# Performance work log

Measured on AMD Instinct MI355X. Metric: run time of the kernel, lower is better.

The kernel has to match this reference:

```python
import jax, jax.numpy as jnp
import numpy as np

NUM_HEAD = 16

def setup_inputs() -> dict:
    rk = jax.random.key(0)
    k1, k2, k3, k4, k5 = jax.random.split(rk, 5)
    B, Sq, Skv, D = 4, 2048, 2048, 1024
    return {
        "query": jax.random.normal(k1, (B, Sq, D), dtype=jnp.float32),
        "key":   jax.random.normal(k2, (B, Skv, D), dtype=jnp.float32),
        "value": jax.random.normal(k3, (B, Skv, D), dtype=jnp.float32),
        "W": jax.random.normal(k4, (D, D), dtype=jnp.float32) * (D ** -0.5),
        "b": jax.random.normal(k5, (D,), dtype=jnp.float32) * 0.01,
    }

def reference(query, key, value, W, b):
    B, Sq, D = query.shape
    H = NUM_HEAD
    hd = D // H
    # chunk(num_head, -1) == split last dim into H contiguous heads
    q = query.reshape(B, Sq, H, hd)
    k = key.reshape(B, -1, H, hd)
    v = value.reshape(B, -1, H, hd)
    # scores[b,h,q,k] = (Q_h K_h^T) / sqrt(embedding_dim)  (full dim, per source)
    scores = jnp.einsum('bqhd,bkhd->bhqk', q, k) / jnp.sqrt(jnp.float32(D))
    # nn.Softmax(dim=1) on a [B, q, kv] matrix -> softmax over the QUERY axis
    attn = jax.nn.softmax(scores, axis=2)
    out = jnp.einsum('bhqk,bkhd->bqhd', attn, v).reshape(B, Sq, D)
    # final linear: x @ W^T + b
    return out @ W.T + b
```

## Files before the change

### kernel.cpp

```cpp
#include <hip/hip_runtime.h>

#define NH    16
#define HD    64
#define SQ    2048
#define SKV   2048
#define DM    1024

typedef __attribute__((ext_vector_type(8))) __bf16 bf16x8;
typedef __attribute__((ext_vector_type(4))) __bf16 bf16x4;
typedef __attribute__((ext_vector_type(4))) float  f32x4;
typedef __attribute__((ext_vector_type(4))) short  s16x4;

#define ASYNC16(gp, lp)                                                        \
    __builtin_amdgcn_global_load_lds(                                          \
        (const __attribute__((address_space(1))) void*)(gp),                   \
        (__attribute__((address_space(3))) void*)(lp), 16, 0, 0)

#if __has_builtin(__builtin_amdgcn_exp2f)
#define EXPS(x) __builtin_amdgcn_exp2f((x) * 0.04508422f)
#else
#define EXPS(x) __expf((x) * 0.03125f)
#endif

#if __has_builtin(__builtin_amdgcn_mfma_f32_16x16x16bf16_1k)
static __device__ __forceinline__ f32x4 mfma16(bf16x4 a, bf16x4 b, f32x4 c) {
    return __builtin_amdgcn_mfma_f32_16x16x16bf16_1k(
        __builtin_bit_cast(s16x4, a), __builtin_bit_cast(s16x4, b), c, 0, 0, 0);
}
#else
static __device__ __forceinline__ f32x4 mfma16(bf16x4 a, bf16x4 b, f32x4 c) {
    asm volatile("s_nop 1\n\tv_mfma_f32_16x16x16_bf16 %0, %1, %2, %0"
                 : "+v"(c) : "v"(a), "v"(b));
    return c;
}
#endif

static __device__ __forceinline__ int swz(int row, int chunk) {
    return (row << 6) + (((chunk) ^ (row & 7)) << 3);
}

static __device__ __forceinline__ bf16x4 cvt4(float4 v) {
    bf16x4 r;
    r[0] = (__bf16)v.x; r[1] = (__bf16)v.y; r[2] = (__bf16)v.z; r[3] = (__bf16)v.w;
    return r;
}

__global__ void kprep_all(const float* __restrict__ q, const float* __restrict__ k,
                          const float* __restrict__ W,
                          __bf16* __restrict__ Qh, __bf16* __restrict__ Kh,
                          __bf16* __restrict__ Wb) {
    int bid = blockIdx.x;
    if (bid < 8192) {
        const float* src = (bid < 4096) ? q : k;
        __bf16* dst = (bid < 4096) ? Qh : Kh;
        size_t g = (size_t)(bid & 4095) * 256 + threadIdx.x;
        size_t o = g * 8;
        int c  = (int)(o & 63);
        int s  = (int)((o >> 6) & 2047);
        int bh = (int)(o >> 17);
        int b = bh >> 4, h = bh & 15;
        const float* p = src + ((size_t)(b * SQ + s)) * DM + h * HD + c;
        float4 v0 = *(const float4*)p;
        float4 v1 = *(const float4*)(p + 4);
        bf16x8 r;
        r[0] = (__bf16)v0.x; r[1] = (__bf16)v0.y; r[2] = (__bf16)v0.z; r[3] = (__bf16)v0.w;
        r[4] = (__bf16)v1.x; r[5] = (__bf16)v1.y; r[6] = (__bf16)v1.z; r[7] = (__bf16)v1.w;
        *(bf16x8*)(dst + o) = r;
    } else {
        int i = (bid - 8192) * 256 + threadIdx.x;
        float4 v = *(const float4*)(W + (size_t)i * 4);
        *(bf16x4*)(Wb + (size_t)i * 4) = cvt4(v);
    }
}

__global__ __launch_bounds__(256, 4) void kz(const __bf16* __restrict__ Qh,
                                             const __bf16* __restrict__ Kh,
                                             const float* __restrict__ v,
                                             __bf16* __restrict__ Vt) {
    const int bh = blockIdx.x;
    const int kb = blockIdx.y;
    const int b = bh >> 4, h = bh & 15;
    const int t = threadIdx.x;
    const int w = t >> 6, lane = t & 63;
    const int lo16 = lane & 15, quad = lane >> 4;
    const int wub = (t & 192) << 3;

    __shared__ __bf16 Ks[128 * 64];
    __shared__ __bf16 Qs[2][64 * 64];
    __shared__ float  Zs[128];

    const __bf16* kbase = Kh + ((size_t)bh * SKV + kb * 128) * HD;
    const __bf16* qbase = Qh + (size_t)bh * SQ * HD;

#pragma unroll
    for (int i = 0; i < 4; ++i) {
        int ci = i * 256 + t;
        int row = ci >> 3;
        int c = (ci & 7) ^ (row & 7);
        ASYNC16(kbase + row * 64 + c * 8, &Ks[i * 2048 + wub]);
    }
#pragma unroll
    for (int i = 0; i < 2; ++i) {
        int ci = i * 256 + t;
        int row = ci >> 3;
        int c = (ci & 7) ^ (row & 7);
        ASYNC16(qbase + row * 64 + c * 8, &Qs[0][i * 2048 + wub]);
    }
    __syncthreads();

    bf16x8 bk[2][2];
#pragma unroll
    for (int nt = 0; nt < 2; ++nt)
#pragma unroll
        for (int dh = 0; dh < 2; ++dh)
            bk[nt][dh] = *(const bf16x8*)(&Ks[swz(w * 32 + nt * 16 + lo16, dh * 4 + quad)]);

    float zacc[2] = {0.f, 0.f};

    for (int qt = 0; qt < 32; ++qt) {
        const int cur = qt & 1, nxt = cur ^ 1;
        if (qt < 31) {
#pragma unroll
            for (int i = 0; i < 2; ++i) {
                int ci = i * 256 + t;
                int row = ci >> 3;
                int c = (ci & 7) ^ (row & 7);
                ASYNC16(qbase + (size_t)(qt + 1) * 64 * HD + row * 64 + c * 8,
                        &Qs[nxt][i * 2048 + wub]);
            }
        }

#pragma unroll
        for (int mt = 0; mt < 4; ++mt) {
            bf16x8 aq0 = *(const bf16x8*)(&Qs[cur][swz(mt * 16 + lo16, quad)]);
            bf16x8 aq1 = *(const bf16x8*)(&Qs[cur][swz(mt * 16 + lo16, 4 + quad)]);
#pragma unroll
            for (int nt = 0; nt < 2; ++nt) {
                f32x4 acc = {0.f, 0.f, 0.f, 0.f};
                acc = __builtin_amdgcn_mfma_f32_16x16x32_bf16(aq0, bk[nt][0], acc, 0, 0, 0);
                acc = __builtin_amdgcn_mfma_f32_16x16x32_bf16(aq1, bk[nt][1], acc, 0, 0, 0);
                zacc[nt] += EXPS(acc[0]) + EXPS(acc[1]) + EXPS(acc[2]) + EXPS(acc[3]);
            }
        }
        __syncthreads();
    }

#pragma unroll
    for (int nt = 0; nt < 2; ++nt) {
        float s = zacc[nt];
        s += __shfl_xor(s, 16, 64);
        s += __shfl_xor(s, 32, 64);
        if (lane < 16) Zs[w * 32 + nt * 16 + lane] = s;
    }
    __syncthreads();

    {
        int kk = t & 127, dh2 = t >> 7;
        float rz = 1.0f / Zs[kk];
        int kfull = kb * 128 + kk;
        const float* vrow = v + ((size_t)(b * SKV) + kfull) * DM + h * HD + dh2 * 32;
        size_t vtb = (size_t)bh * HD * SKV + (size_t)(dh2 * 32) * SKV + kfull;
#pragma unroll
        for (int dc = 0; dc < 2; ++dc) {
            float4 a0 = *(const float4*)(vrow + dc * 16 + 0);
            float4 a1 = *(const float4*)(vrow + dc * 16 + 4);
            float4 a2 = *(const float4*)(vrow + dc * 16 + 8);
            float4 a3 = *(const float4*)(vrow + dc * 16 + 12);
            float tmp[16] = {a0.x, a0.y, a0.z, a0.w, a1.x, a1.y, a1.z, a1.w,
                             a2.x, a2.y, a2.z, a2.w, a3.x, a3.y, a3.z, a3.w};
#pragma unroll
            for (int j = 0; j < 16; ++j)
                Vt[vtb + (size_t)(dc * 16 + j) * SKV] = (__bf16)(tmp[j] * rz);
        }
    }
}

__global__ __launch_bounds__(256, 2) void kattn(const __bf16* __restrict__ Qh,
                                                const __bf16* __restrict__ Kh,
                                                const __bf16* __restrict__ Vt,
                                                __bf16* __restrict__ O) {
    const int bh = blockIdx.x;
    const int qb = blockIdx.y;
    const int b = bh >> 4, h = bh & 15;
    const int t = threadIdx.x;
    const int w = t >> 6, lane = t & 63;
    const int lo16 = lane & 15, quad = lane >> 4;
    const int wub = (t & 192) << 3;

    __shared__ __bf16 Ks[2][64 * 64];
    __shared__ __bf16 Vts[2][64 * 64];
    __shared__ __bf16 Qstage[256 * 64];

    const __bf16* qgbase = Qh + ((size_t)bh * SQ + qb * 256) * HD;
    const __bf16* kgbase = Kh + (size_t)bh * SKV * HD;
    const __bf16* vtgbase = Vt + (size_t)bh * HD * SKV;

#pragma unroll
    for (int i = 0; i < 8; ++i) {
        int ci = i * 256 + t;
        int row = ci >> 3;
        int c = (ci & 7) ^ (row & 7);
        ASYNC16(qgbase + row * 64 + c * 8, &Qstage[i * 2048 + wub]);
    }
#pragma unroll
    for (int i = 0; i < 2; ++i) {
        int ci = i * 256 + t;
        int row = ci >> 3;
        int c = (ci & 7) ^ (row & 7);
        ASYNC16(kgbase + row * 64 + c * 8, &Ks[0][i * 2048 + wub]);
        ASYNC16(vtgbase + (size_t)row * SKV + c * 8, &Vts[0][i * 2048 + wub]);
    }
    __syncthreads();

    bf16x8 qf[4][2];
#pragma unroll
    for (int qt = 0; qt < 4; ++qt)
#pragma unroll
        for (int dh = 0; dh < 2; ++dh)
            qf[qt][dh] = *(const bf16x8*)(&Qstage[swz(w * 64 + qt * 16 + lo16, dh * 4 + quad)]);

    f32x4 oacc[4][4];
    f32x4 zero = {0.f, 0.f, 0.f, 0.f};
#pragma unroll
    for (int qt = 0; qt < 4; ++qt)
#pragma unroll
        for (int nt = 0; nt < 4; ++nt)
            oacc[qt][nt] = zero;

    for (int kt = 0; kt < 32; ++kt) {
        const int cur = kt & 1, nxt = cur ^ 1;
        if (kt < 31) {
#pragma unroll
            for (int i = 0; i < 2; ++i) {
                int ci = i * 256 + t;
                int row = ci >> 3;
                int c = (ci & 7) ^ (row & 7);
                ASYNC16(kgbase + (size_t)(kt + 1) * 64 * HD + row * 64 + c * 8,
                        &Ks[nxt][i * 2048 + wub]);
                ASYNC16(vtgbase + (size_t)row * SKV + (kt + 1) * 64 + c * 8,
                        &Vts[nxt][i * 2048 + wub]);
            }
        }

        bf16x4 ef[4][4];
#pragma unroll
        for (int kg = 0; kg < 4; ++kg) {
            bf16x8 ak0 = *(const bf16x8*)(&Ks[cur][swz(kg * 16 + lo16, quad)]);
            bf16x8 ak1 = *(const bf16x8*)(&Ks[cur][swz(kg * 16 + lo16, 4 + quad)]);
#pragma unroll
            for (int qt = 0; qt < 4; ++qt) {
                f32x4 s = zero;
                s = __builtin_amdgcn_mfma_f32_16x16x32_bf16(ak0, qf[qt][0], s, 0, 0, 0);
                s = __builtin_amdgcn_mfma_f32_16x16x32_bf16(ak1, qf[qt][1], s, 0, 0, 0);
                bf16x4 e;
                e[0] = (__bf16)EXPS(s[0]);
                e[1] = (__bf16)EXPS(s[1]);
                e[2] = (__bf16)EXPS(s[2]);
                e[3] = (__bf16)EXPS(s[3]);
                ef[qt][kg] = e;
            }
        }

#pragma unroll
        for (int nt = 0; nt < 4; ++nt) {
#pragma unroll
            for (int kg = 0; kg < 4; ++kg) {
                int row = nt * 16 + lo16;
                int chunk = kg * 2 + (quad >> 1);
                bf16x4 bv = *(const bf16x4*)(
                    &Vts[cur][(row << 6) + ((chunk ^ (row & 7)) << 3) + ((quad & 1) << 2)]);
#pragma unroll
                for (int qt = 0; qt < 4; ++qt)
                    oacc[qt][nt] = mfma16(ef[qt][kg], bv, oacc[qt][nt]);
            }
        }
        __syncthreads();
    }

    asm volatile("s_nop 7\n\ts_nop 7" ::: );

    size_t obase = ((size_t)(b * SQ) + qb * 256 + w * 64) * DM + h * HD;
#pragma unroll
    for (int qt = 0; qt < 4; ++qt)
#pragma unroll
        for (int nt = 0; nt < 4; ++nt)
#pragma unroll
            for (int r = 0; r < 4; ++r)
                O[obase + (size_t)(qt * 16 + quad * 4 + r) * DM + nt * 16 + lo16] =
                    (__bf16)oacc[qt][nt][r];
}

__global__ __launch_bounds__(256, 2) void kproj(const __bf16* __restrict__ A,
                                                const __bf16* __restrict__ Wb,
                                                const float* __restrict__ bias,
                                                float* __restrict__ out) {
    const int nb = blockIdx.x;
    const int mb = blockIdx.y;
    const int t = threadIdx.x;
    const int w = t >> 6, lane = t & 63;
    const int lo16 = lane & 15, quad = lane >> 4;
    const int wm = w & 1, wn = w >> 1;
    const int wub = (t & 192) << 3;

    __shared__ __bf16 As[2][128 * 64];
    __shared__ __bf16 Bs[2][128 * 64];

    f32x4 acc[4][4];
    f32x4 zero = {0.f, 0.f, 0.f, 0.f};
#pragma unroll
    for (int mt = 0; mt < 4; ++mt)
#pragma unroll
        for (int nt = 0; nt < 4; ++nt)
            acc[mt][nt] = zero;

    const __bf16* abase = A + (size_t)(mb * 128) * DM;
    const __bf16* wbase = Wb + (size_t)(nb * 128) * DM;

#pragma unroll
    for (int i = 0; i < 4; ++i) {
        int ci = i * 256 + t;
        int row = ci >> 3;
        int c = (ci & 7) ^ (row & 7);
        ASYNC16(abase + (size_t)row * DM + c * 8, &As[0][i * 2048 + wub]);
        ASYNC16(wbase + (size_t)row * DM + c * 8, &Bs[0][i * 2048 + wub]);
    }
    __syncthreads();

    for (int kt = 0; kt < 16; ++kt) {
        const int cur = kt & 1, nxt = cur ^ 1;
        if (kt < 15) {
#pragma unroll
            for (int i = 0; i < 4; ++i) {
                int ci = i * 256 + t;
                int row = ci >> 3;
                int c = (ci & 7) ^ (row & 7);
                ASYNC16(abase + (size_t)row * DM + (kt + 1) * 64 + c * 8, &As[nxt][i * 2048 + wub]);
                ASYNC16(wbase + (size_t)row * DM + (kt + 1) * 64 + c * 8, &Bs[nxt][i * 2048 + wub]);
            }
        }

#pragma unroll
        for (int ks = 0; ks < 2; ++ks) {
            bf16x8 av[4], bv[4];
#pragma unroll
            for (int mt = 0; mt < 4; ++mt)
                av[mt] = *(const bf16x8*)(&As[cur][swz(wm * 64 + mt * 16 + lo16, ks * 4 + quad)]);
#pragma unroll
            for (int nt = 0; nt < 4; ++nt)
                bv[nt] = *(const bf16x8*)(&Bs[cur][swz(wn * 64 + nt * 16 + lo16, ks * 4 + quad)]);
#pragma unroll
            for (int mt = 0; mt < 4; ++mt)
#pragma unroll
                for (int nt = 0; nt < 4; ++nt)
                    acc[mt][nt] = __builtin_amdgcn_mfma_f32_16x16x32_bf16(av[mt], bv[nt], acc[mt][nt], 0, 0, 0);
        }
        __syncthreads();
    }

    const int col0 = nb * 128 + wn * 64;
    const int row0 = mb * 128 + wm * 64;
#pragma unroll
    for (int nt = 0; nt < 4; ++nt) {
        float bb = bias[col0 + nt * 16 + lo16];
#pragma unroll
        for (int mt = 0; mt < 4; ++mt)
#pragma unroll
            for (int r = 0; r < 4; ++r)
                out[(size_t)(row0 + mt * 16 + quad * 4 + r) * DM + col0 + nt * 16 + lo16] =
                    acc[mt][nt][r] + bb;
    }
}

extern "C" void kernel_launch(void* const* d_in, const int* in_sizes, int n_in,
                              void* d_out, int out_size, void* d_ws, size_t ws_size,
                              hipStream_t stream) {
    const float* q    = (const float*)d_in[0];
    const float* k    = (const float*)d_in[1];
    const float* v    = (const float*)d_in[2];
    const float* W    = (const float*)d_in[3];
    const float* bias = (const float*)d_in[4];
    float* out = (float*)d_out;

    char* ws = (char*)d_ws;
    __bf16* Qh = (__bf16*)ws;
    __bf16* Kh = (__bf16*)(ws + (16u << 20));
    __bf16* Vt = (__bf16*)(ws + (32u << 20));
    __bf16* Wb = (__bf16*)(ws + (48u << 20));
    __bf16* O  = (__bf16*)(ws + (50u << 20));

    kprep_all<<<dim3(9216), 256, 0, stream>>>(q, k, W, Qh, Kh, Wb);
    kz       <<<dim3(64, 16), 256, 0, stream>>>(Qh, Kh, v, Vt);
    kattn    <<<dim3(64, 8), 256, 0, stream>>>(Qh, Kh, Vt, O);
    kproj    <<<dim3(8, 64), 256, 0, stream>>>(O, Wb, bias, out);
}
```

Baseline: 298.3 us.

## Load Q/K/V fragments directly from global into registers, drop LDS staging

The z-normalizer and attention kernels now read their MFMA operand fragments straight from global memory into registers, using ping-pong register buffers as software prefetch, instead of staging tiles in LDS with async copies and block barriers. In the attention kernel the exponentiated scores are written to a per-wave LDS region and re-read as 8-wide operands, so the PV product uses the 16x16x32 MFMA instead of the 16x16x16 one. This removes the __syncthreads per tile and the LDS staging traffic. The cost is uncoalesced global fragment loads that rely on L2/L1 reuse across waves, and higher register pressure.

```diff
diff --git a/kernel.cpp b/kernel.cpp
--- a/kernel.cpp
+++ b/kernel.cpp
@@ -9,7 +9,6 @@
 typedef __attribute__((ext_vector_type(8))) __bf16 bf16x8;
 typedef __attribute__((ext_vector_type(4))) __bf16 bf16x4;
 typedef __attribute__((ext_vector_type(4))) float  f32x4;
-typedef __attribute__((ext_vector_type(4))) short  s16x4;
 
 #define ASYNC16(gp, lp)                                                        \
     __builtin_amdgcn_global_load_lds(                                          \
@@ -20,19 +19,6 @@
 #define EXPS(x) __builtin_amdgcn_exp2f((x) * 0.04508422f)
 #else
 #define EXPS(x) __expf((x) * 0.03125f)
-#endif
-
-#if __has_builtin(__builtin_amdgcn_mfma_f32_16x16x16bf16_1k)
-static __device__ __forceinline__ f32x4 mfma16(bf16x4 a, bf16x4 b, f32x4 c) {
-    return __builtin_amdgcn_mfma_f32_16x16x16bf16_1k(
-        __builtin_bit_cast(s16x4, a), __builtin_bit_cast(s16x4, b), c, 0, 0, 0);
-}
-#else
-static __device__ __forceinline__ f32x4 mfma16(bf16x4 a, bf16x4 b, f32x4 c) {
-    asm volatile("s_nop 1\n\tv_mfma_f32_16x16x16_bf16 %0, %1, %2, %0"
-                 : "+v"(c) : "v"(a), "v"(b));
-    return c;
-}
 #endif
 
 static __device__ __forceinline__ int swz(int row, int chunk) {
@@ -83,66 +69,53 @@
     const int t = threadIdx.x;
     const int w = t >> 6, lane = t & 63;
     const int lo16 = lane & 15, quad = lane >> 4;
-    const int wub = (t & 192) << 3;
-
-    __shared__ __bf16 Ks[128 * 64];
-    __shared__ __bf16 Qs[2][64 * 64];
-    __shared__ float  Zs[128];
+
+    __shared__ float Zs[128];
 
     const __bf16* kbase = Kh + ((size_t)bh * SKV + kb * 128) * HD;
     const __bf16* qbase = Qh + (size_t)bh * SQ * HD;
 
-#pragma unroll
-    for (int i = 0; i < 4; ++i) {
-        int ci = i * 256 + t;
-        int row = ci >> 3;
-        int c = (ci & 7) ^ (row & 7);
-        ASYNC16(kbase + row * 64 + c * 8, &Ks[i * 2048 + wub]);
-    }
-#pragma unroll
-    for (int i = 0; i < 2; ++i) {
-        int ci = i * 256 + t;
-        int row = ci >> 3;
-        int c = (ci & 7) ^ (row & 7);
-        ASYNC16(qbase + row * 64 + c * 8, &Qs[0][i * 2048 + wub]);
-    }
-    __syncthreads();
-
     bf16x8 bk[2][2];
 #pragma unroll
     for (int nt = 0; nt < 2; ++nt)
 #pragma unroll
         for (int dh = 0; dh < 2; ++dh)
-            bk[nt][dh] = *(const bf16x8*)(&Ks[swz(w * 32 + nt * 16 + lo16, dh * 4 + quad)]);
+            bk[nt][dh] = *(const bf16x8*)(kbase + (size_t)(w * 32 + nt * 16 + lo16) * HD
+                                          + dh * 32 + quad * 8);
 
     float zacc[2] = {0.f, 0.f};
 
-    for (int qt = 0; qt < 32; ++qt) {
-        const int cur = qt & 1, nxt = cur ^ 1;
-        if (qt < 31) {
-#pragma unroll
-            for (int i = 0; i < 2; ++i) {
-                int ci = i * 256 + t;
-                int row = ci >> 3;
-                int c = (ci & 7) ^ (row & 7);
-                ASYNC16(qbase + (size_t)(qt + 1) * 64 * HD + row * 64 + c * 8,
-                        &Qs[nxt][i * 2048 + wub]);
-            }
-        }
-
+    bf16x8 aqA[4][2], aqB[4][2];
+#pragma unroll
+    for (int mt = 0; mt < 4; ++mt)
+#pragma unroll
+        for (int dh = 0; dh < 2; ++dh)
+            aqA[mt][dh] = *(const bf16x8*)(qbase + (size_t)(mt * 16 + lo16) * HD
+                                           + dh * 32 + quad * 8);
+
+    auto kz_tile = [&](bf16x8 (&aqc)[4][2], bf16x8 (&aqn)[4][2], int qtn) {
+#pragma unroll
+        for (int mt = 0; mt < 4; ++mt)
+#pragma unroll
+            for (int dh = 0; dh < 2; ++dh)
+                aqn[mt][dh] = *(const bf16x8*)(qbase
+                    + (size_t)(qtn * 64 + mt * 16 + lo16) * HD + dh * 32 + quad * 8);
 #pragma unroll
         for (int mt = 0; mt < 4; ++mt) {
-            bf16x8 aq0 = *(const bf16x8*)(&Qs[cur][swz(mt * 16 + lo16, quad)]);
-            bf16x8 aq1 = *(const bf16x8*)(&Qs[cur][swz(mt * 16 + lo16, 4 + quad)]);
 #pragma unroll
             for (int nt = 0; nt < 2; ++nt) {
                 f32x4 acc = {0.f, 0.f, 0.f, 0.f};
-                acc = __builtin_amdgcn_mfma_f32_16x16x32_bf16(aq0, bk[nt][0], acc, 0, 0, 0);
-                acc = __builtin_amdgcn_mfma_f32_16x16x32_bf16(aq1, bk[nt][1], acc, 0, 0, 0);
+                acc = __builtin_amdgcn_mfma_f32_16x16x32_bf16(aqc[mt][0], bk[nt][0], acc, 0, 0, 0);
+                acc = __builtin_amdgcn_mfma_f32_16x16x32_bf16(aqc[mt][1], bk[nt][1], acc, 0, 0, 0);
                 zacc[nt] += EXPS(acc[0]) + EXPS(acc[1]) + EXPS(acc[2]) + EXPS(acc[3]);
             }
         }
-        __syncthreads();
+    };
+
+    for (int qt2 = 0; qt2 < 16; ++qt2) {
+        int qt = qt2 * 2;
+        kz_tile(aqA, aqB, qt + 1);
+        kz_tile(aqB, aqA, (qt + 2 < 32) ? qt + 2 : 31);
     }
 
 #pragma unroll
@@ -185,39 +158,20 @@
     const int t = threadIdx.x;
     const int w = t >> 6, lane = t & 63;
     const int lo16 = lane & 15, quad = lane >> 4;
-    const int wub = (t & 192) << 3;
-
-    __shared__ __bf16 Ks[2][64 * 64];
-    __shared__ __bf16 Vts[2][64 * 64];
-    __shared__ __bf16 Qstage[256 * 64];
-
-    const __bf16* qgbase = Qh + ((size_t)bh * SQ + qb * 256) * HD;
-    const __bf16* kgbase = Kh + (size_t)bh * SKV * HD;
-    const __bf16* vtgbase = Vt + (size_t)bh * HD * SKV;
-
-#pragma unroll
-    for (int i = 0; i < 8; ++i) {
-        int ci = i * 256 + t;
-        int row = ci >> 3;
-        int c = (ci & 7) ^ (row & 7);
-        ASYNC16(qgbase + row * 64 + c * 8, &Qstage[i * 2048 + wub]);
-    }
-#pragma unroll
-    for (int i = 0; i < 2; ++i) {
-        int ci = i * 256 + t;
-        int row = ci >> 3;
-        int c = (ci & 7) ^ (row & 7);
-        ASYNC16(kgbase + row * 64 + c * 8, &Ks[0][i * 2048 + wub]);
-        ASYNC16(vtgbase + (size_t)row * SKV + c * 8, &Vts[0][i * 2048 + wub]);
-    }
-    __syncthreads();
+
+    __shared__ __bf16 Es[4 * 64 * 64];
+
+    const __bf16* qg  = Qh + ((size_t)bh * SQ + qb * 256) * HD;
+    const __bf16* kgl = Kh + (size_t)bh * SKV * HD;
+    const __bf16* vtg = Vt + (size_t)bh * HD * SKV;
 
     bf16x8 qf[4][2];
 #pragma unroll
     for (int qt = 0; qt < 4; ++qt)
 #pragma unroll
         for (int dh = 0; dh < 2; ++dh)
-            qf[qt][dh] = *(const bf16x8*)(&Qstage[swz(w * 64 + qt * 16 + lo16, dh * 4 + quad)]);
+            qf[qt][dh] = *(const bf16x8*)(qg + (size_t)(w * 64 + qt * 16 + lo16) * HD
+                                          + dh * 32 + quad * 8);
 
     f32x4 oacc[4][4];
     f32x4 zero = {0.f, 0.f, 0.f, 0.f};
@@ -227,57 +181,67 @@
         for (int nt = 0; nt < 4; ++nt)
             oacc[qt][nt] = zero;
 
-    for (int kt = 0; kt < 32; ++kt) {
-        const int cur = kt & 1, nxt = cur ^ 1;
-        if (kt < 31) {
-#pragma unroll
-            for (int i = 0; i < 2; ++i) {
-                int ci = i * 256 + t;
-                int row = ci >> 3;
-                int c = (ci & 7) ^ (row & 7);
-                ASYNC16(kgbase + (size_t)(kt + 1) * 64 * HD + row * 64 + c * 8,
-                        &Ks[nxt][i * 2048 + wub]);
-                ASYNC16(vtgbase + (size_t)row * SKV + (kt + 1) * 64 + c * 8,
-                        &Vts[nxt][i * 2048 + wub]);
-            }
-        }
-
-        bf16x4 ef[4][4];
+    __bf16* Ew = &Es[w * 4096];
+
+    bf16x8 akA[4][2], akB[4][2];
+#pragma unroll
+    for (int kg = 0; kg < 4; ++kg)
+#pragma unroll
+        for (int dh = 0; dh < 2; ++dh)
+            akA[kg][dh] = *(const bf16x8*)(kgl + (size_t)(kg * 16 + lo16) * HD
+                                           + dh * 32 + quad * 8);
+
+    auto attn_tile = [&](bf16x8 (&akc)[4][2], bf16x8 (&akn)[4][2], int kt, int ktn) {
+        bf16x8 bv[2][4];
+#pragma unroll
+        for (int kk2 = 0; kk2 < 2; ++kk2)
+#pragma unroll
+            for (int nt = 0; nt < 4; ++nt)
+                bv[kk2][nt] = *(const bf16x8*)(vtg + (size_t)(nt * 16 + lo16) * SKV
+                                               + kt * 64 + kk2 * 32 + quad * 8);
 #pragma unroll
         for (int kg = 0; kg < 4; ++kg) {
-            bf16x8 ak0 = *(const bf16x8*)(&Ks[cur][swz(kg * 16 + lo16, quad)]);
-            bf16x8 ak1 = *(const bf16x8*)(&Ks[cur][swz(kg * 16 + lo16, 4 + quad)]);
 #pragma unroll
             for (int qt = 0; qt < 4; ++qt) {
                 f32x4 s = zero;
-                s = __builtin_amdgcn_mfma_f32_16x16x32_bf16(ak0, qf[qt][0], s, 0, 0, 0);
-                s = __builtin_amdgcn_mfma_f32_16x16x32_bf16(ak1, qf[qt][1], s, 0, 0, 0);
+                s = __builtin_amdgcn_mfma_f32_16x16x32_bf16(akc[kg][0], qf[qt][0], s, 0, 0, 0);
+                s = __builtin_amdgcn_mfma_f32_16x16x32_bf16(akc[kg][1], qf[qt][1], s, 0, 0, 0);
                 bf16x4 e;
                 e[0] = (__bf16)EXPS(s[0]);
                 e[1] = (__bf16)EXPS(s[1]);
                 e[2] = (__bf16)EXPS(s[2]);
                 e[3] = (__bf16)EXPS(s[3]);
-                ef[qt][kg] = e;
+                int er = qt * 16 + lo16;
+                *(bf16x4*)(&Ew[(er << 6) + (((2 * kg + (quad >> 1)) ^ (er & 7)) << 3)
+                               + (quad & 1) * 4]) = e;
             }
         }
-
-#pragma unroll
-        for (int nt = 0; nt < 4; ++nt) {
-#pragma unroll
-            for (int kg = 0; kg < 4; ++kg) {
-                int row = nt * 16 + lo16;
-                int chunk = kg * 2 + (quad >> 1);
-                bf16x4 bv = *(const bf16x4*)(
-                    &Vts[cur][(row << 6) + ((chunk ^ (row & 7)) << 3) + ((quad & 1) << 2)]);
+#pragma unroll
+        for (int kg = 0; kg < 4; ++kg)
+#pragma unroll
+            for (int dh = 0; dh < 2; ++dh)
+                akn[kg][dh] = *(const bf16x8*)(kgl + (size_t)(ktn * 64 + kg * 16 + lo16) * HD
+                                               + dh * 32 + quad * 8);
+#pragma unroll
+        for (int kk2 = 0; kk2 < 2; ++kk2) {
+            bf16x8 ae[4];
+#pragma unroll
+            for (int qt = 0; qt < 4; ++qt)
+                ae[qt] = *(const bf16x8*)(&Ew[swz(qt * 16 + lo16, kk2 * 4 + quad)]);
+#pragma unroll
+            for (int nt = 0; nt < 4; ++nt)
 #pragma unroll
                 for (int qt = 0; qt < 4; ++qt)
-                    oacc[qt][nt] = mfma16(ef[qt][kg], bv, oacc[qt][nt]);
-            }
-        }
-        __syncthreads();
-    }
-
-    asm volatile("s_nop 7\n\ts_nop 7" ::: );
+                    oacc[qt][nt] = __builtin_amdgcn_mfma_f32_16x16x32_bf16(
+                        ae[qt], bv[kk2][nt], oacc[qt][nt], 0, 0, 0);
+        }
+    };
+
+    for (int kt2 = 0; kt2 < 16; ++kt2) {
+        int kt = kt2 * 2;
+        attn_tile(akA, akB, kt, kt + 1);
+        attn_tile(akB, akA, kt + 1, (kt + 2 < 32) ? kt + 2 : 31);
+    }
 
     size_t obase = ((size_t)(b * SQ) + qb * 256 + w * 64) * DM + h * HD;
 #pragma unroll
```

Result: slower. 425.4 us (+42.6%).
